# Kernel tuning notes

Measured on AMD Instinct MI355X. Metric: run time of the kernel, lower is better.

## Reference

```python
import jax, jax.numpy as jnp
import numpy as np

H, L, N = 128, 8192, 64


def setup_inputs() -> dict:
    key = jax.random.key(0)
    ks = jax.random.split(key, 8)
    u = jax.random.normal(ks[0], (H, L), jnp.float32)
    # lecun_normal-scaled params, per channel
    Ct_ri = jax.random.normal(ks[1], (H, N, 2), jnp.float32) / np.sqrt(N)
    B_raw = jax.random.normal(ks[2], (H, N, 1), jnp.float32) / np.sqrt(N)
    D = jax.random.uniform(ks[3], (H,), jnp.float32)
    lo, hi = np.log(0.001), np.log(0.1)
    log_step = jax.random.uniform(ks[4], (H,), jnp.float32) * (hi - lo) + lo
    n = np.arange(N, dtype=np.float32)
    Lambda_re = jnp.full((N,), -0.5, jnp.float32)
    Lambda_im = jnp.asarray(np.pi * n, jnp.float32)
    p_re = jnp.asarray(np.sqrt(n + 0.5), jnp.float32)
    p_im = jnp.zeros((N,), jnp.float32)
    q_re = jnp.asarray(np.sqrt(n + 0.5), jnp.float32)
    q_im = jnp.zeros((N,), jnp.float32)
    Vc_re = jax.random.normal(ks[5], (N, N), jnp.float32) / np.sqrt(N)
    Vc_im = jax.random.normal(ks[6], (N, N), jnp.float32) / np.sqrt(N)
    return dict(u=u, Ct_ri=Ct_ri, B_raw=B_raw, D=D, log_step=log_step,
                Lambda_re=Lambda_re, Lambda_im=Lambda_im,
                p_re=p_re, p_im=p_im, q_re=q_re, q_im=q_im,
                Vc_re=Vc_re, Vc_im=Vc_im)


def _s4_forward(u, Ct_ri, B_raw, D, log_step,
                Lambda_re, Lambda_im, p_re, p_im, q_re, q_im, Vc_re, Vc_im):
    h, l = u.shape
    Lambda = (Lambda_re + 1j * Lambda_im).astype(jnp.complex64)   # (N,)
    p = (p_re + 1j * p_im).astype(jnp.complex64)                  # (N,)
    q = (q_re + 1j * q_im).astype(jnp.complex64)                  # (N,)
    Vc = (Vc_re + 1j * Vc_im).astype(jnp.complex64)               # (N,N)
    Ct = (Ct_ri[..., 0] + 1j * Ct_ri[..., 1]).astype(jnp.complex64)  # (H,N)
    # B = Vc @ B_raw  per channel -> (H,N)
    B = jnp.einsum('nm,hm->hn', Vc, B_raw[..., 0].astype(jnp.complex64))
    step = jnp.exp(log_step)                                      # (H,)

    # K_gen_DPLR evaluated at the L roots of unity (conv_from_gen)
    omega = jnp.exp(-2j * jnp.pi * (jnp.arange(l) / l)).astype(jnp.complex64)  # (L,)
    g = (2.0 / step)[:, None] * ((1.0 - omega) / (1.0 + omega))[None, :]       # (H,L)
    c = 2.0 / (1.0 + omega)                                                    # (L,)

    # cauchy_dot: sum_n a_n / (g - Lambda_n); reuse one (H,L,N) reciprocal
    recip = 1.0 / (g[:, :, None] - Lambda[None, None, :])          # (H,L,N)
    Ctc = Ct.conj()
    k00 = jnp.einsum('hn,hln->hl', Ctc * B, recip)
    k01 = jnp.einsum('hn,hln->hl', Ctc * p[None, :], recip)
    k10 = jnp.einsum('hn,hln->hl', q.conj()[None, :] * B, recip)
    k11 = jnp.einsum('n,hln->hl', q.conj() * p, recip)
    at_roots = c[None, :] * (k00 - k01 * (1.0 / (1.0 + k11)) * k10)  # (H,L)

    K = jnp.fft.ifft(at_roots, n=l, axis=-1).real                 # (H,L)

    # non_circular_convolution via zero-padded rfft
    ud = jnp.fft.rfft(jnp.pad(u, ((0, 0), (0, l))), axis=-1)
    Kd = jnp.fft.rfft(jnp.pad(K, ((0, 0), (0, l))), axis=-1)
    y = jnp.fft.irfft(ud * Kd, axis=-1)[:, :l]                    # (H,L)
    return y + D[:, None] * u


def reference(u, Ct_ri, B_raw, D, log_step,
              Lambda_re, Lambda_im, p_re, p_im, q_re, q_im, Vc_re, Vc_im):
    return _s4_forward(u, Ct_ri, B_raw, D, log_step,
                       Lambda_re, Lambda_im, p_re, p_im, q_re, q_im,
                       Vc_re, Vc_im)
```

## Files before the change

### kernel.cpp

```cpp
#include <hip/hip_runtime.h>
#include <math.h>

#define H 128
#define L 8192
#define NSTATE 64
#define NTH 1024
#define PI_D 3.14159265358979323846
#define RT2 0.70710678118654752440f

#define W16K_RE 0.99999992646571789f
#define W16K_IM (-3.8349518757139556e-4f)
#define W32K_RE 0.99999998161642898f
#define W32K_IM (-1.9174759731070332e-4f)

typedef float v2f __attribute__((ext_vector_type(2)));

__device__ __forceinline__ v2f pkfma(v2f a, v2f b, v2f c) {
    return __builtin_elementwise_fma(a, b, c);
}
__device__ __forceinline__ v2f pkfma(float a, v2f b, v2f c) {
    v2f av = a; return __builtin_elementwise_fma(av, b, c);
}

__device__ __forceinline__ int SWZ(int e) { return e ^ ((e >> 3) & 7); }
__device__ __forceinline__ int TSW(int j) { return j ^ ((j >> 4) & 15) ^ ((j >> 8) & 15); }
__device__ __forceinline__ int brev13(int x) { return (int)(__brev((unsigned)x) >> 19); }

__device__ __forceinline__ float2 cmul(float2 a, float2 b) {
    return make_float2(a.x * b.x - a.y * b.y, a.x * b.y + a.y * b.x);
}
__device__ __forceinline__ float2 cmulc(float2 w, float2 x) {
    return make_float2(w.x * x.x + w.y * x.y, w.x * x.y - w.y * x.x);
}
__device__ __forceinline__ float2 cadd(float2 a, float2 b) { return make_float2(a.x + b.x, a.y + b.y); }
__device__ __forceinline__ float2 csub(float2 a, float2 b) { return make_float2(a.x - b.x, a.y - b.y); }
__device__ __forceinline__ float2 mnegi(float2 a) { return make_float2(a.y, -a.x); }
__device__ __forceinline__ float2 mposi(float2 a) { return make_float2(-a.y, a.x); }

template<int SIGMA>
__device__ __forceinline__ void dif_r8(float2* __restrict__ A,
                                       const float2* __restrict__ tw, int tid) {
    const int M1 = 1024 / SIGMA;
    int r = tid & (SIGMA - 1);
    int b = ((tid & ~(SIGMA - 1)) << 3) | r;
    float2 w1 = tw[TSW(r * M1)];
    float2 w2 = cmul(w1, w1);
    float2 w4 = cmul(w2, w2);
    float2 wj1 = cmul(w1, make_float2(RT2, -RT2));
    float2 wj2 = mnegi(w1);
    float2 wj3 = cmul(w1, make_float2(-RT2, -RT2));
    int i0 = SWZ(b), i1 = SWZ(b + SIGMA), i2 = SWZ(b + 2 * SIGMA), i3 = SWZ(b + 3 * SIGMA);
    int i4 = SWZ(b + 4 * SIGMA), i5 = SWZ(b + 5 * SIGMA), i6 = SWZ(b + 6 * SIGMA), i7 = SWZ(b + 7 * SIGMA);
    float2 x0 = A[i0], x1 = A[i1], x2 = A[i2], x3 = A[i3];
    float2 x4 = A[i4], x5 = A[i5], x6 = A[i6], x7 = A[i7];
    float2 a0 = cadd(x0, x4), a1 = cadd(x1, x5), a2 = cadd(x2, x6), a3 = cadd(x3, x7);
    float2 s0 = cmul(csub(x0, x4), w1);
    float2 s1 = cmul(csub(x1, x5), wj1);
    float2 s2 = cmul(csub(x2, x6), wj2);
    float2 s3 = cmul(csub(x3, x7), wj3);
    float2 c0 = cadd(a0, a2), c1 = cadd(a1, a3);
    float2 c2 = cmul(csub(a0, a2), w2);
    float2 c3 = cmul(mnegi(csub(a1, a3)), w2);
    float2 d0 = cadd(s0, s2), d1 = cadd(s1, s3);
    float2 d2 = cmul(csub(s0, s2), w2);
    float2 d3 = cmul(mnegi(csub(s1, s3)), w2);
    A[i0] = cadd(c0, c1); A[i1] = cmul(csub(c0, c1), w4);
    A[i2] = cadd(c2, c3); A[i3] = cmul(csub(c2, c3), w4);
    A[i4] = cadd(d0, d1); A[i5] = cmul(csub(d0, d1), w4);
    A[i6] = cadd(d2, d3); A[i7] = cmul(csub(d2, d3), w4);
}

template<int SIGMA>
__device__ __forceinline__ void dit_r8(float2* __restrict__ A,
                                       const float2* __restrict__ tw, int tid) {
    const int M1 = 1024 / SIGMA;
    int r = tid & (SIGMA - 1);
    int b = ((tid & ~(SIGMA - 1)) << 3) | r;
    float2 w1 = tw[TSW(r * M1)];
    float2 w2 = cmul(w1, w1);
    float2 w4 = cmul(w2, w2);
    float2 wj1 = cmul(w1, make_float2(RT2, -RT2));
    float2 wj2 = mnegi(w1);
    float2 wj3 = cmul(w1, make_float2(-RT2, -RT2));
    int i0 = SWZ(b), i1 = SWZ(b + SIGMA), i2 = SWZ(b + 2 * SIGMA), i3 = SWZ(b + 3 * SIGMA);
    int i4 = SWZ(b + 4 * SIGMA), i5 = SWZ(b + 5 * SIGMA), i6 = SWZ(b + 6 * SIGMA), i7 = SWZ(b + 7 * SIGMA);
    float2 x0 = A[i0], x1 = A[i1], x2 = A[i2], x3 = A[i3];
    float2 x4 = A[i4], x5 = A[i5], x6 = A[i6], x7 = A[i7];
    float2 t;
    t = cmulc(w4, x1); float2 e0 = cadd(x0, t), e1 = csub(x0, t);
    t = cmulc(w4, x3); float2 e2 = cadd(x2, t), e3 = csub(x2, t);
    t = cmulc(w4, x5); float2 e4 = cadd(x4, t), e5 = csub(x4, t);
    t = cmulc(w4, x7); float2 e6 = cadd(x6, t), e7 = csub(x6, t);
    t = cmulc(w2, e2);        float2 f0 = cadd(e0, t), f2 = csub(e0, t);
    t = mposi(cmulc(w2, e3)); float2 f1 = cadd(e1, t), f3 = csub(e1, t);
    t = cmulc(w2, e6);        float2 f4 = cadd(e4, t), f6 = csub(e4, t);
    t = mposi(cmulc(w2, e7)); float2 f5 = cadd(e5, t), f7 = csub(e5, t);
    t = cmulc(w1, f4);  A[i0] = cadd(f0, t); A[i4] = csub(f0, t);
    t = cmulc(wj1, f5); A[i1] = cadd(f1, t); A[i5] = csub(f1, t);
    t = cmulc(wj2, f6); A[i2] = cadd(f2, t); A[i6] = csub(f2, t);
    t = cmulc(wj3, f7); A[i3] = cadd(f3, t); A[i7] = csub(f3, t);
}

__device__ __forceinline__ void dif_first_load(float2* __restrict__ A,
                                               const float2* __restrict__ tw,
                                               int tid, const float* __restrict__ ur,
                                               int type) {
    #pragma unroll
    for (int rep = 0; rep < 2; ++rep) {
        int q = tid + rep * NTH;
        float u0 = ur[q], u1 = ur[q + 2048], u2v = ur[q + 4096], u3v = ur[q + 6144];
        float2 x0, x1, x2, x3;
        if (type == 0) {
            x0 = make_float2(u0, 0.f); x1 = make_float2(u1, 0.f);
            x2 = make_float2(u2v, 0.f); x3 = make_float2(u3v, 0.f);
        } else {
            int hq = q >> 1;
            float2 wa = tw[TSW(hq)];
            float2 wb = tw[TSW(hq + 1024)];
            float2 adj = (q & 1) ? make_float2(W16K_RE, W16K_IM) : make_float2(1.f, 0.f);
            wa = cmul(wa, adj); wb = cmul(wb, adj);
            float2 wc = mnegi(wa), wd = mnegi(wb);
            x0 = make_float2(u0 * wa.x, u0 * wa.y);
            x1 = make_float2(u1 * wb.x, u1 * wb.y);
            x2 = make_float2(u2v * wc.x, u2v * wc.y);
            x3 = make_float2(u3v * wd.x, u3v * wd.y);
        }
        float2 w1 = tw[TSW(q)];
        float2 w2 = cmul(w1, w1);
        float2 w1b = mnegi(w1);
        float2 y0 = cadd(x0, x2), y2 = cmul(csub(x0, x2), w1);
        float2 y1 = cadd(x1, x3), y3 = cmul(csub(x1, x3), w1b);
        A[SWZ(q)]        = cadd(y0, y1);
        A[SWZ(q + 2048)] = cmul(csub(y0, y1), w2);
        A[SWZ(q + 4096)] = cadd(y2, y3);
        A[SWZ(q + 6144)] = cmul(csub(y2, y3), w2);
    }
}

template<bool SP>
__device__ __forceinline__ void dit_last_store(const float2* __restrict__ A,
                                               const float2* __restrict__ tw,
                                               int tid, int type,
                                               const float* __restrict__ ur, float Dh,
                                               float* __restrict__ orow,
                                               float* __restrict__ yrow) {
    const float sc = 0.5f / (float)L;
    #pragma unroll
    for (int rep = 0; rep < 2; ++rep) {
        int q = tid + rep * NTH;
        float2 v1 = tw[TSW(q)];
        float2 v2 = cmul(v1, v1);
        float2 x0 = A[SWZ(q)], x1 = A[SWZ(q + 2048)];
        float2 x2 = A[SWZ(q + 4096)], x3 = A[SWZ(q + 6144)];
        float2 t1 = cmulc(v2, x1);
        float2 y0 = cadd(x0, t1), y1 = csub(x0, t1);
        float2 t3 = cmulc(v2, x3);
        float2 y2 = cadd(x2, t3), y3 = csub(x2, t3);
        float2 u2c = cmulc(v1, y2);
        float2 z0 = cadd(y0, u2c), z2 = csub(y0, u2c);
        float2 u3c = mposi(cmulc(v1, y3));
        float2 z1 = cadd(y1, u3c), z3 = csub(y1, u3c);
        float v0, vv1, vv2, vv3;
        if (type == 0) {
            v0  = z0.x * sc + Dh * ur[q];
            vv1 = z1.x * sc + Dh * ur[q + 2048];
            vv2 = z2.x * sc + Dh * ur[q + 4096];
            vv3 = z3.x * sc + Dh * ur[q + 6144];
        } else {
            int hq = q >> 1;
            float2 wa = tw[TSW(hq)];
            float2 wb = tw[TSW(hq + 1024)];
            float2 adj = (q & 1) ? make_float2(W16K_RE, W16K_IM) : make_float2(1.f, 0.f);
            wa = cmul(wa, adj); wb = cmul(wb, adj);
            float2 wc = mnegi(wa), wd = mnegi(wb);
            v0  = (wa.x * z0.x + wa.y * z0.y) * sc;
            vv1 = (wb.x * z1.x + wb.y * z1.y) * sc;
            vv2 = (wc.x * z2.x + wc.y * z2.y) * sc;
            vv3 = (wd.x * z3.x + wd.y * z3.y) * sc;
        }
        float* dst = (type == 0) ? orow : (SP ? yrow : orow);
        if constexpr (SP) {
            dst[q] = v0; dst[q + 2048] = vv1; dst[q + 4096] = vv2; dst[q + 6144] = vv3;
        } else {
            atomicAdd(&dst[q], v0); atomicAdd(&dst[q + 2048], vv1);
            atomicAdd(&dst[q + 4096], vv2); atomicAdd(&dst[q + 6144], vv3);
        }
    }
}

template<int P>
__device__ __forceinline__ void cauchy_chunk(
    const int type, const int tid, const float two_over_step,
    const float2* __restrict__ tw,
    const float4* __restrict__ wq, const float2* __restrict__ wr,
    const float4* __restrict__ wp,
    float* __restrict__ specRe, float* __restrict__ specIm)
{
    const float2 W16K = make_float2(W16K_RE, W16K_IM);
    const float2 W32K = make_float2(W32K_RE, W32K_IM);
    float tk0, tk1;
    v2f gv;
    #pragma unroll
    for (int e = 0; e < 2; ++e) {
        int k = brev13(8 * tid + 2 * P + e);
        float2 w;
        if (e == 0) {
            w = tw[TSW(k >> 1)];
        } else {
            float2 t0 = tw[TSW((k >> 1) - 2048)];
            w = make_float2(t0.y, -t0.x);
        }
        if (k & 1) w = cmul(w, W16K);
        if (type)  w = cmul(w, W32K);
        float t = -w.y * __builtin_amdgcn_rcpf(w.x);
        t = fminf(fmaxf(t, -3.0e7f), 3.0e7f);
        if (e == 0) { tk0 = t; gv.x = two_over_step * t; }
        else        { tk1 = t; gv.y = two_over_step * t; }
    }
    v2f A00x = 0.f, A00y = 0.f, A01x = 0.f, A01y = 0.f;
    v2f A10x = 0.f, A10y = 0.f, A11x = 0.f, A11y = 0.f;
    #pragma unroll 2
    for (int n = 0; n < NSTATE; ++n) {
        float4 qv = wq[n];
        float2 rv = wr[n];
        float4 pv = wp[n];
        v2f dim = gv - pv.z;
        v2f dre2 = pv.y;
        v2f den = pkfma(dim, dim, dre2);
        float rp = __builtin_amdgcn_rcpf(den.x * den.y);
        v2f inv; inv.x = den.y * rp; inv.y = den.x * rp;
        v2f rre = pv.x * inv;
        v2f rip = dim * inv;
        A00x = pkfma(qv.x, rre, pkfma( qv.y, rip, A00x));
        A00y = pkfma(qv.y, rre, pkfma(-qv.x, rip, A00y));
        A01x = pkfma(qv.z, rre, pkfma( qv.w, rip, A01x));
        A01y = pkfma(qv.w, rre, pkfma(-qv.z, rip, A01y));
        A10x = pkfma(rv.x, rre, pkfma( rv.y, rip, A10x));
        A10y = pkfma(rv.y, rre, pkfma(-rv.x, rip, A10y));
        A11x = pkfma( pv.w, rre, A11x);
        A11y = pkfma(-pv.w, rip, A11y);
    }
    #pragma unroll
    for (int e = 0; e < 2; ++e) {
        float2 a00 = make_float2(e ? A00x.y : A00x.x, e ? A00y.y : A00y.x);
        float2 a01 = make_float2(e ? A01x.y : A01x.x, e ? A01y.y : A01y.x);
        float2 a10 = make_float2(e ? A10x.y : A10x.x, e ? A10y.y : A10y.x);
        float2 a11 = make_float2(e ? A11x.y : A11x.x, e ? A11y.y : A11y.x);
        float tt = e ? tk1 : tk0;
        float2 den1 = make_float2(1.0f + a11.x, a11.y);
        float invd = 1.0f / (den1.x * den1.x + den1.y * den1.y);
        float2 qn = cmul(a01, a10);
        float2 dv = make_float2((qn.x * den1.x + qn.y * den1.y) * invd,
                                (qn.y * den1.x - qn.x * den1.y) * invd);
        float2 tmp = make_float2(a00.x - dv.x, a00.y - dv.y);
        float2 s = cmul(make_float2(1.0f, tt), tmp);
        int j = 2 * P + e;
        specRe[j * NTH + tid] = s.x;
        specIm[j * NTH + tid] = s.y;
    }
}

__global__ __launch_bounds__(NSTATE)
void s4_prep(const float* __restrict__ Ct_ri, const float* __restrict__ B_raw,
             const float* __restrict__ Lre_g, const float* __restrict__ Lim_g,
             const float* __restrict__ p_re, const float* __restrict__ p_im,
             const float* __restrict__ q_re, const float* __restrict__ q_im,
             const float* __restrict__ Vc_re, const float* __restrict__ Vc_im,
             char* __restrict__ ws)
{
    const int h = blockIdx.x, n = threadIdx.x;
    float2 Bc = make_float2(0.f, 0.f);
    for (int m = 0; m < NSTATE; ++m) {
        float br = B_raw[h * NSTATE + m];
        Bc.x += Vc_re[n * NSTATE + m] * br;
        Bc.y += Vc_im[n * NSTATE + m] * br;
    }
    float2 Ctc = make_float2(Ct_ri[(h * NSTATE + n) * 2 + 0],
                             -Ct_ri[(h * NSTATE + n) * 2 + 1]);
    float2 pc = make_float2(p_re[n], p_im[n]);
    float2 qc = make_float2(q_re[n], -q_im[n]);
    float2 w00 = cmul(Ctc, Bc);
    float2 w01 = cmul(Ctc, pc);
    float2 w10 = cmul(qc, Bc);
    float2 w11 = cmul(qc, pc);
    float dre = -Lre_g[n];
    float4* wq = (float4*)ws;
    float2* wr = (float2*)(ws + (size_t)H * NSTATE * 16);
    float4* wp = (float4*)(ws + (size_t)H * NSTATE * 24);
    wq[h * NSTATE + n] = make_float4(w00.x, w00.y, w01.x, w01.y);
    wr[h * NSTATE + n] = make_float2(w10.x, w10.y);
    wp[h * NSTATE + n] = make_float4(dre, dre * dre, Lim_g[n], w11.x);
}

__global__ __launch_bounds__(256)
void s4_combine(float4* __restrict__ out, const float4* __restrict__ yneg) {
    int i = blockIdx.x * 256 + threadIdx.x;
    float4 a = out[i], b = yneg[i];
    out[i] = make_float4(a.x + b.x, a.y + b.y, a.z + b.z, a.w + b.w);
}

extern __shared__ char smem_raw[];

template<bool WG, bool SP>
__global__ __launch_bounds__(NTH)
void s4_split_kernel(const float* __restrict__ u,
                     const float* __restrict__ Ct_ri,
                     const float* __restrict__ B_raw,
                     const float* __restrict__ Dp,
                     const float* __restrict__ log_step,
                     const float* __restrict__ Lre_g,
                     const float* __restrict__ Lim_g,
                     const float* __restrict__ p_re,
                     const float* __restrict__ p_im,
                     const float* __restrict__ q_re,
                     const float* __restrict__ q_im,
                     const float* __restrict__ Vc_re,
                     const float* __restrict__ Vc_im,
                     const char* __restrict__ wsw,
                     float* __restrict__ yneg,
                     float* __restrict__ out)
{
    float2* bufA   = (float2*)smem_raw;
    float2* tw     = bufA + L;
    float*  specRe = (float*)(tw + 2048);
    float*  specIm = specRe + L;
    float4* wq4    = (float4*)(specIm + L);
    float2* wr2    = (float2*)(wq4 + NSTATE);
    float4* wp4    = (float4*)(wr2 + NSTATE);

    const int bid  = blockIdx.x;
    const int type = bid >> 7;
    const int h    = bid & (H - 1);
    const int tid  = threadIdx.x;

    for (int j = tid; j < 2048; j += NTH) {
        double a = -2.0 * PI_D * (double)j / (double)L;
        tw[TSW(j)] = make_float2((float)cos(a), (float)sin(a));
    }
    const float4* wqp; const float2* wrp; const float4* wpp;
    if constexpr (WG) {
        wqp = (const float4*)wsw + (size_t)h * NSTATE;
        wrp = (const float2*)(wsw + (size_t)H * NSTATE * 16) + (size_t)h * NSTATE;
        wpp = (const float4*)(wsw + (size_t)H * NSTATE * 24) + (size_t)h * NSTATE;
    } else {
        if (tid < NSTATE) {
            int n = tid;
            float2 Bc = make_float2(0.f, 0.f);
            for (int m = 0; m < NSTATE; ++m) {
                float br = B_raw[h * NSTATE + m];
                Bc.x += Vc_re[n * NSTATE + m] * br;
                Bc.y += Vc_im[n * NSTATE + m] * br;
            }
            float2 Ctc = make_float2(Ct_ri[(h * NSTATE + n) * 2 + 0],
                                     -Ct_ri[(h * NSTATE + n) * 2 + 1]);
            float2 pc = make_float2(p_re[n], p_im[n]);
            float2 qc = make_float2(q_re[n], -q_im[n]);
            float2 w00 = cmul(Ctc, Bc);
            float2 w01 = cmul(Ctc, pc);
            float2 w10 = cmul(qc, Bc);
            float2 w11 = cmul(qc, pc);
            float dre = -Lre_g[n];
            wq4[n] = make_float4(w00.x, w00.y, w01.x, w01.y);
            wr2[n] = make_float2(w10.x, w10.y);
            wp4[n] = make_float4(dre, dre * dre, Lim_g[n], w11.x);
        }
        wqp = wq4; wrp = wr2; wpp = wp4;
    }
    __syncthreads();

    const float step = expf(log_step[h]);
    const float two_over_step = 2.0f / step;
    const float Dh = Dp[h];
    const float* ur = u + (size_t)h * L;

    dif_first_load(bufA, tw, tid, ur, type);
    cauchy_chunk<0>(type, tid, two_over_step, tw, wqp, wrp, wpp, specRe, specIm);
    __syncthreads();
    dif_r8<256>(bufA, tw, tid);
    cauchy_chunk<1>(type, tid, two_over_step, tw, wqp, wrp, wpp, specRe, specIm);
    __syncthreads();
    dif_r8<32>(bufA, tw, tid);
    cauchy_chunk<2>(type, tid, two_over_step, tw, wqp, wrp, wpp, specRe, specIm);
    __syncthreads();
    dif_r8<4>(bufA, tw, tid);
    cauchy_chunk<3>(type, tid, two_over_step, tw, wqp, wrp, wpp, specRe, specIm);
    __syncthreads();

    {
        const int base = tid * 8;
        #pragma unroll
        for (int un = 0; un < 2; ++un) {
            int p0 = base + un * 4;
            int j0 = SWZ(p0), j1 = SWZ(p0 + 1), j2 = SWZ(p0 + 2), j3 = SWZ(p0 + 3);
            float2 x0 = bufA[j0], x1 = bufA[j1], x2 = bufA[j2], x3 = bufA[j3];
            float2 a0 = cadd(x0, x2), a1 = cadd(x1, x3);
            float2 s0 = csub(x0, x2), s1 = mnegi(csub(x1, x3));
            float2 y0 = cadd(a0, a1), y1 = csub(a0, a1);
            float2 y2 = cadd(s0, s1), y3 = csub(s0, s1);
            int sj = un * 4;
            y0 = cmul(y0, make_float2(specRe[(sj + 0) * NTH + tid], specIm[(sj + 0) * NTH + tid]));
            y1 = cmul(y1, make_float2(specRe[(sj + 1) * NTH + tid], specIm[(sj + 1) * NTH + tid]));
            y2 = cmul(y2, make_float2(specRe[(sj + 2) * NTH + tid], specIm[(sj + 2) * NTH + tid]));
            y3 = cmul(y3, make_float2(specRe[(sj + 3) * NTH + tid], specIm[(sj + 3) * NTH + tid]));
            float2 e0 = cadd(y0, y1), e1 = csub(y0, y1);
            float2 e2 = cadd(y2, y3), e3 = csub(y2, y3);
            float2 ti = mposi(e3);
            bufA[j0] = cadd(e0, e2); bufA[j2] = csub(e0, e2);
            bufA[j1] = cadd(e1, ti); bufA[j3] = csub(e1, ti);
        }
    }
    __syncthreads();

    dit_r8<4>(bufA, tw, tid);   __syncthreads();
    dit_r8<32>(bufA, tw, tid);  __syncthreads();
    dit_r8<256>(bufA, tw, tid); __syncthreads();
    dit_last_store<SP>(bufA, tw, tid, type, ur, Dh,
                       out + (size_t)h * L,
                       SP ? (yneg + (size_t)h * L) : nullptr);
}

extern "C" void kernel_launch(void* const* d_in, const int* in_sizes, int n_in,
                              void* d_out, int out_size, void* d_ws, size_t ws_size,
                              hipStream_t stream) {
    (void)in_sizes; (void)n_in; (void)out_size;
    const float* u        = (const float*)d_in[0];
    const float* Ct_ri    = (const float*)d_in[1];
    const float* B_raw    = (const float*)d_in[2];
    const float* Dp       = (const float*)d_in[3];
    const float* log_step = (const float*)d_in[4];
    const float* Lre      = (const float*)d_in[5];
    const float* Lim      = (const float*)d_in[6];
    const float* p_re     = (const float*)d_in[7];
    const float* p_im     = (const float*)d_in[8];
    const float* q_re     = (const float*)d_in[9];
    const float* q_im     = (const float*)d_in[10];
    const float* Vc_re    = (const float*)d_in[11];
    const float* Vc_im    = (const float*)d_in[12];
    float* out = (float*)d_out;

    const size_t needW = (size_t)H * NSTATE * (16 + 8 + 16);
    const size_t needY = needW + (size_t)H * L * sizeof(float);
    const bool wg = ws_size >= needW;
    const bool sp = ws_size >= needY;

    char*  wsw  = (char*)d_ws;
    float* yneg = (float*)((char*)d_ws + needW);

    const size_t smemW = (size_t)(L + 2048) * sizeof(float2)
                       + (size_t)2 * L * sizeof(float);
    const size_t smemL = smemW + NSTATE * (16 + 8 + 16);

    if (wg) {
        s4_prep<<<dim3(H), dim3(NSTATE), 0, stream>>>(
            Ct_ri, B_raw, Lre, Lim, p_re, p_im, q_re, q_im, Vc_re, Vc_im, wsw);
        if (sp) {
            hipFuncSetAttribute((const void*)s4_split_kernel<true, true>,
                                hipFuncAttributeMaxDynamicSharedMemorySize, (int)smemW);
            s4_split_kernel<true, true><<<dim3(2 * H), dim3(NTH), smemW, stream>>>(
                u, Ct_ri, B_raw, Dp, log_step, Lre, Lim,
                p_re, p_im, q_re, q_im, Vc_re, Vc_im, wsw, yneg, out);
            s4_combine<<<dim3((H * L) / (256 * 4)), dim3(256), 0, stream>>>(
                (float4*)out, (const float4*)yneg);
        } else {
            hipMemsetAsync(out, 0, (size_t)H * L * sizeof(float), stream);
            hipFuncSetAttribute((const void*)s4_split_kernel<true, false>,
                                hipFuncAttributeMaxDynamicSharedMemorySize, (int)smemW);
            s4_split_kernel<true, false><<<dim3(2 * H), dim3(NTH), smemW, stream>>>(
                u, Ct_ri, B_raw, Dp, log_step, Lre, Lim,
                p_re, p_im, q_re, q_im, Vc_re, Vc_im, wsw, nullptr, out);
        }
    } else {
        hipMemsetAsync(out, 0, (size_t)H * L * sizeof(float), stream);
        hipFuncSetAttribute((const void*)s4_split_kernel<false, false>,
                            hipFuncAttributeMaxDynamicSharedMemorySize, (int)smemL);
        s4_split_kernel<false, false><<<dim3(2 * H), dim3(NTH), smemL, stream>>>(
            u, Ct_ri, B_raw, Dp, log_step, Lre, Lim,
            p_re, p_im, q_re, q_im, Vc_re, Vc_im, nullptr, nullptr, out);
    }
}
```

Baseline: 77.86 us.

## Restructure 8192-point FFT into radix-16/8/8/8 passes to cut LDS stages

Replaces the radix-4 first/last FFT passes plus four radix-8 passes with a radix-16 first/last pass (run by 512 threads) and radix-8 middle stages, moving the pointwise spectrum multiply into a full radix-8 butterfly. This removes one LDS round trip and one block barrier on each of the forward and inverse sides. In exchange, half the threads idle during the radix-16 passes, those threads carry 16 complex values in registers, and constant-memory twiddle tables are added.

```diff
diff --git a/kernel.cpp b/kernel.cpp
--- a/kernel.cpp
+++ b/kernel.cpp
@@ -36,6 +36,35 @@
 __device__ __forceinline__ float2 csub(float2 a, float2 b) { return make_float2(a.x - b.x, a.y - b.y); }
 __device__ __forceinline__ float2 mnegi(float2 a) { return make_float2(a.y, -a.x); }
 __device__ __forceinline__ float2 mposi(float2 a) { return make_float2(-a.y, a.x); }
+
+__device__ __constant__ float2 C16[8] = {
+    { 1.f, 0.f },
+    { 0.9238795325112867f, -0.3826834323650898f },
+    { 0.7071067811865476f, -0.7071067811865476f },
+    { 0.3826834323650898f, -0.9238795325112867f },
+    { 0.f, -1.f },
+    { -0.3826834323650898f, -0.9238795325112867f },
+    { -0.7071067811865476f, -0.7071067811865476f },
+    { -0.9238795325112867f, -0.3826834323650898f },
+};
+__device__ __constant__ float2 C32[16] = {
+    { 1.f, 0.f },
+    { 0.9807852804032304f, -0.1950903220161283f },
+    { 0.9238795325112867f, -0.3826834323650898f },
+    { 0.8314696123025452f, -0.5555702330196022f },
+    { 0.7071067811865476f, -0.7071067811865476f },
+    { 0.5555702330196022f, -0.8314696123025452f },
+    { 0.3826834323650898f, -0.9238795325112867f },
+    { 0.1950903220161283f, -0.9807852804032304f },
+    { 0.f, -1.f },
+    { -0.1950903220161283f, -0.9807852804032304f },
+    { -0.3826834323650898f, -0.9238795325112867f },
+    { -0.5555702330196022f, -0.8314696123025452f },
+    { -0.7071067811865476f, -0.7071067811865476f },
+    { -0.8314696123025452f, -0.5555702330196022f },
+    { -0.9238795325112867f, -0.3826834323650898f },
+    { -0.9807852804032304f, -0.1950903220161283f },
+};
 
 template<int SIGMA>
 __device__ __forceinline__ void dif_r8(float2* __restrict__ A,
@@ -101,89 +130,126 @@
     t = cmulc(wj3, f7); A[i3] = cadd(f3, t); A[i7] = csub(f3, t);
 }
 
-__device__ __forceinline__ void dif_first_load(float2* __restrict__ A,
-                                               const float2* __restrict__ tw,
-                                               int tid, const float* __restrict__ ur,
-                                               int type) {
-    #pragma unroll
-    for (int rep = 0; rep < 2; ++rep) {
-        int q = tid + rep * NTH;
-        float u0 = ur[q], u1 = ur[q + 2048], u2v = ur[q + 4096], u3v = ur[q + 6144];
-        float2 x0, x1, x2, x3;
-        if (type == 0) {
-            x0 = make_float2(u0, 0.f); x1 = make_float2(u1, 0.f);
-            x2 = make_float2(u2v, 0.f); x3 = make_float2(u3v, 0.f);
-        } else {
-            int hq = q >> 1;
-            float2 wa = tw[TSW(hq)];
-            float2 wb = tw[TSW(hq + 1024)];
-            float2 adj = (q & 1) ? make_float2(W16K_RE, W16K_IM) : make_float2(1.f, 0.f);
-            wa = cmul(wa, adj); wb = cmul(wb, adj);
-            float2 wc = mnegi(wa), wd = mnegi(wb);
-            x0 = make_float2(u0 * wa.x, u0 * wa.y);
-            x1 = make_float2(u1 * wb.x, u1 * wb.y);
-            x2 = make_float2(u2v * wc.x, u2v * wc.y);
-            x3 = make_float2(u3v * wd.x, u3v * wd.y);
-        }
-        float2 w1 = tw[TSW(q)];
-        float2 w2 = cmul(w1, w1);
-        float2 w1b = mnegi(w1);
-        float2 y0 = cadd(x0, x2), y2 = cmul(csub(x0, x2), w1);
-        float2 y1 = cadd(x1, x3), y3 = cmul(csub(x1, x3), w1b);
-        A[SWZ(q)]        = cadd(y0, y1);
-        A[SWZ(q + 2048)] = cmul(csub(y0, y1), w2);
-        A[SWZ(q + 4096)] = cadd(y2, y3);
-        A[SWZ(q + 6144)] = cmul(csub(y2, y3), w2);
-    }
+__device__ __forceinline__ void dif_first16(float2* __restrict__ A,
+                                            const float2* __restrict__ tw,
+                                            int t, const float* __restrict__ ur,
+                                            int type) {
+    float2 x[16];
+    if (type == 0) {
+        #pragma unroll
+        for (int j = 0; j < 16; ++j) x[j] = make_float2(ur[t + 512 * j], 0.f);
+    } else {
+        float2 wt = tw[TSW(t >> 1)];
+        if (t & 1) wt = cmul(wt, make_float2(W16K_RE, W16K_IM));
+        #pragma unroll
+        for (int j = 0; j < 16; ++j) {
+            float2 wj = cmul(wt, C32[j]);
+            float uv = ur[t + 512 * j];
+            x[j] = make_float2(uv * wj.x, uv * wj.y);
+        }
+    }
+    float2 w1 = tw[TSW(t)];
+    float2 w2 = cmul(w1, w1);
+    float2 w4 = cmul(w2, w2);
+    float2 w8 = cmul(w4, w4);
+    #pragma unroll
+    for (int j = 0; j < 8; ++j) {
+        float2 wj = cmul(w1, C16[j]);
+        float2 a = cadd(x[j], x[j + 8]);
+        float2 b = cmul(csub(x[j], x[j + 8]), wj);
+        x[j] = a; x[j + 8] = b;
+    }
+    #pragma unroll
+    for (int g = 0; g < 16; g += 8)
+        #pragma unroll
+        for (int j = 0; j < 4; ++j) {
+            float2 wj = cmul(w2, C16[2 * j]);
+            float2 a = cadd(x[g + j], x[g + j + 4]);
+            float2 b = cmul(csub(x[g + j], x[g + j + 4]), wj);
+            x[g + j] = a; x[g + j + 4] = b;
+        }
+    #pragma unroll
+    for (int g = 0; g < 16; g += 4) {
+        { float2 a = cadd(x[g], x[g + 2]);
+          float2 b = cmul(csub(x[g], x[g + 2]), w4);
+          x[g] = a; x[g + 2] = b; }
+        { float2 a = cadd(x[g + 1], x[g + 3]);
+          float2 b = cmul(csub(x[g + 1], x[g + 3]), mnegi(w4));
+          x[g + 1] = a; x[g + 3] = b; }
+    }
+    #pragma unroll
+    for (int g = 0; g < 16; g += 2) {
+        float2 a = cadd(x[g], x[g + 1]);
+        float2 b = cmul(csub(x[g], x[g + 1]), w8);
+        x[g] = a; x[g + 1] = b;
+    }
+    #pragma unroll
+    for (int j = 0; j < 16; ++j) A[SWZ(t + 512 * j)] = x[j];
 }
 
 template<bool SP>
-__device__ __forceinline__ void dit_last_store(const float2* __restrict__ A,
-                                               const float2* __restrict__ tw,
-                                               int tid, int type,
-                                               const float* __restrict__ ur, float Dh,
-                                               float* __restrict__ orow,
-                                               float* __restrict__ yrow) {
+__device__ __forceinline__ void dit_last16(const float2* __restrict__ A,
+                                           const float2* __restrict__ tw,
+                                           int t, int type,
+                                           const float* __restrict__ ur, float Dh,
+                                           float* __restrict__ orow,
+                                           float* __restrict__ yrow) {
+    float2 x[16];
+    #pragma unroll
+    for (int j = 0; j < 16; ++j) x[j] = A[SWZ(t + 512 * j)];
+    float2 w1 = tw[TSW(t)];
+    float2 w2 = cmul(w1, w1);
+    float2 w4 = cmul(w2, w2);
+    float2 w8 = cmul(w4, w4);
+    #pragma unroll
+    for (int g = 0; g < 16; g += 2) {
+        float2 tt = cmulc(w8, x[g + 1]);
+        float2 a = cadd(x[g], tt), b = csub(x[g], tt);
+        x[g] = a; x[g + 1] = b;
+    }
+    #pragma unroll
+    for (int g = 0; g < 16; g += 4) {
+        { float2 tt = cmulc(w4, x[g + 2]);
+          float2 a = cadd(x[g], tt), b = csub(x[g], tt);
+          x[g] = a; x[g + 2] = b; }
+        { float2 tt = mposi(cmulc(w4, x[g + 3]));
+          float2 a = cadd(x[g + 1], tt), b = csub(x[g + 1], tt);
+          x[g + 1] = a; x[g + 3] = b; }
+    }
+    #pragma unroll
+    for (int g = 0; g < 16; g += 8)
+        #pragma unroll
+        for (int j = 0; j < 4; ++j) {
+            float2 wj = cmul(w2, C16[2 * j]);
+            float2 tt = cmulc(wj, x[g + j + 4]);
+            float2 a = cadd(x[g + j], tt), b = csub(x[g + j], tt);
+            x[g + j] = a; x[g + j + 4] = b;
+        }
+    #pragma unroll
+    for (int j = 0; j < 8; ++j) {
+        float2 wj = cmul(w1, C16[j]);
+        float2 tt = cmulc(wj, x[j + 8]);
+        float2 a = cadd(x[j], tt), b = csub(x[j], tt);
+        x[j] = a; x[j + 8] = b;
+    }
     const float sc = 0.5f / (float)L;
-    #pragma unroll
-    for (int rep = 0; rep < 2; ++rep) {
-        int q = tid + rep * NTH;
-        float2 v1 = tw[TSW(q)];
-        float2 v2 = cmul(v1, v1);
-        float2 x0 = A[SWZ(q)], x1 = A[SWZ(q + 2048)];
-        float2 x2 = A[SWZ(q + 4096)], x3 = A[SWZ(q + 6144)];
-        float2 t1 = cmulc(v2, x1);
-        float2 y0 = cadd(x0, t1), y1 = csub(x0, t1);
-        float2 t3 = cmulc(v2, x3);
-        float2 y2 = cadd(x2, t3), y3 = csub(x2, t3);
-        float2 u2c = cmulc(v1, y2);
-        float2 z0 = cadd(y0, u2c), z2 = csub(y0, u2c);
-        float2 u3c = mposi(cmulc(v1, y3));
-        float2 z1 = cadd(y1, u3c), z3 = csub(y1, u3c);
-        float v0, vv1, vv2, vv3;
-        if (type == 0) {
-            v0  = z0.x * sc + Dh * ur[q];
-            vv1 = z1.x * sc + Dh * ur[q + 2048];
-            vv2 = z2.x * sc + Dh * ur[q + 4096];
-            vv3 = z3.x * sc + Dh * ur[q + 6144];
-        } else {
-            int hq = q >> 1;
-            float2 wa = tw[TSW(hq)];
-            float2 wb = tw[TSW(hq + 1024)];
-            float2 adj = (q & 1) ? make_float2(W16K_RE, W16K_IM) : make_float2(1.f, 0.f);
-            wa = cmul(wa, adj); wb = cmul(wb, adj);
-            float2 wc = mnegi(wa), wd = mnegi(wb);
-            v0  = (wa.x * z0.x + wa.y * z0.y) * sc;
-            vv1 = (wb.x * z1.x + wb.y * z1.y) * sc;
-            vv2 = (wc.x * z2.x + wc.y * z2.y) * sc;
-            vv3 = (wd.x * z3.x + wd.y * z3.y) * sc;
-        }
-        float* dst = (type == 0) ? orow : (SP ? yrow : orow);
-        if constexpr (SP) {
-            dst[q] = v0; dst[q + 2048] = vv1; dst[q + 4096] = vv2; dst[q + 6144] = vv3;
-        } else {
-            atomicAdd(&dst[q], v0); atomicAdd(&dst[q + 2048], vv1);
-            atomicAdd(&dst[q + 4096], vv2); atomicAdd(&dst[q + 6144], vv3);
+    if (type == 0) {
+        #pragma unroll
+        for (int j = 0; j < 16; ++j) {
+            int p = t + 512 * j;
+            float val = x[j].x * sc + Dh * ur[p];
+            if constexpr (SP) orow[p] = val; else atomicAdd(&orow[p], val);
+        }
+    } else {
+        float2 wt = tw[TSW(t >> 1)];
+        if (t & 1) wt = cmul(wt, make_float2(W16K_RE, W16K_IM));
+        float* dst = SP ? yrow : orow;
+        #pragma unroll
+        for (int j = 0; j < 16; ++j) {
+            int p = t + 512 * j;
+            float2 wj = cmul(wt, C32[j]);
+            float val = (wj.x * x[j].x + wj.y * x[j].y) * sc;
+            if constexpr (SP) dst[p] = val; else atomicAdd(&dst[p], val);
         }
     }
 }
@@ -373,48 +439,66 @@
     const float Dh = Dp[h];
     const float* ur = u + (size_t)h * L;
 
-    dif_first_load(bufA, tw, tid, ur, type);
+    if (tid < 512) dif_first16(bufA, tw, tid, ur, type);
     cauchy_chunk<0>(type, tid, two_over_step, tw, wqp, wrp, wpp, specRe, specIm);
     __syncthreads();
-    dif_r8<256>(bufA, tw, tid);
+    dif_r8<64>(bufA, tw, tid);
     cauchy_chunk<1>(type, tid, two_over_step, tw, wqp, wrp, wpp, specRe, specIm);
     __syncthreads();
-    dif_r8<32>(bufA, tw, tid);
+    dif_r8<8>(bufA, tw, tid);
     cauchy_chunk<2>(type, tid, two_over_step, tw, wqp, wrp, wpp, specRe, specIm);
-    __syncthreads();
-    dif_r8<4>(bufA, tw, tid);
     cauchy_chunk<3>(type, tid, two_over_step, tw, wqp, wrp, wpp, specRe, specIm);
     __syncthreads();
 
     {
         const int base = tid * 8;
-        #pragma unroll
-        for (int un = 0; un < 2; ++un) {
-            int p0 = base + un * 4;
-            int j0 = SWZ(p0), j1 = SWZ(p0 + 1), j2 = SWZ(p0 + 2), j3 = SWZ(p0 + 3);
-            float2 x0 = bufA[j0], x1 = bufA[j1], x2 = bufA[j2], x3 = bufA[j3];
-            float2 a0 = cadd(x0, x2), a1 = cadd(x1, x3);
-            float2 s0 = csub(x0, x2), s1 = mnegi(csub(x1, x3));
-            float2 y0 = cadd(a0, a1), y1 = csub(a0, a1);
-            float2 y2 = cadd(s0, s1), y3 = csub(s0, s1);
-            int sj = un * 4;
-            y0 = cmul(y0, make_float2(specRe[(sj + 0) * NTH + tid], specIm[(sj + 0) * NTH + tid]));
-            y1 = cmul(y1, make_float2(specRe[(sj + 1) * NTH + tid], specIm[(sj + 1) * NTH + tid]));
-            y2 = cmul(y2, make_float2(specRe[(sj + 2) * NTH + tid], specIm[(sj + 2) * NTH + tid]));
-            y3 = cmul(y3, make_float2(specRe[(sj + 3) * NTH + tid], specIm[(sj + 3) * NTH + tid]));
-            float2 e0 = cadd(y0, y1), e1 = csub(y0, y1);
-            float2 e2 = cadd(y2, y3), e3 = csub(y2, y3);
-            float2 ti = mposi(e3);
-            bufA[j0] = cadd(e0, e2); bufA[j2] = csub(e0, e2);
-            bufA[j1] = cadd(e1, ti); bufA[j3] = csub(e1, ti);
-        }
+        float2 x0 = bufA[SWZ(base + 0)], x1 = bufA[SWZ(base + 1)];
+        float2 x2 = bufA[SWZ(base + 2)], x3 = bufA[SWZ(base + 3)];
+        float2 x4 = bufA[SWZ(base + 4)], x5 = bufA[SWZ(base + 5)];
+        float2 x6 = bufA[SWZ(base + 6)], x7 = bufA[SWZ(base + 7)];
+        float2 a0 = cadd(x0, x4), a1 = cadd(x1, x5), a2 = cadd(x2, x6), a3 = cadd(x3, x7);
+        float2 s0 = csub(x0, x4), s1 = csub(x1, x5), s2 = csub(x2, x6), s3 = csub(x3, x7);
+        float2 b0 = s0;
+        float2 b1 = cmul(s1, make_float2(RT2, -RT2));
+        float2 b2 = mnegi(s2);
+        float2 b3 = cmul(s3, make_float2(-RT2, -RT2));
+        float2 c0 = cadd(a0, a2), c2 = csub(a0, a2);
+        float2 c1 = cadd(a1, a3), c3 = mnegi(csub(a1, a3));
+        float2 d0 = cadd(b0, b2), d2 = csub(b0, b2);
+        float2 d1 = cadd(b1, b3), d3 = mnegi(csub(b1, b3));
+        float2 y0 = cadd(c0, c1), y1 = csub(c0, c1);
+        float2 y2 = cadd(c2, c3), y3 = csub(c2, c3);
+        float2 y4 = cadd(d0, d1), y5 = csub(d0, d1);
+        float2 y6 = cadd(d2, d3), y7 = csub(d2, d3);
+        y0 = cmul(y0, make_float2(specRe[0 * NTH + tid], specIm[0 * NTH + tid]));
+        y1 = cmul(y1, make_float2(specRe[1 * NTH + tid], specIm[1 * NTH + tid]));
+        y2 = cmul(y2, make_float2(specRe[2 * NTH + tid], specIm[2 * NTH + tid]));
+        y3 = cmul(y3, make_float2(specRe[3 * NTH + tid], specIm[3 * NTH + tid]));
+        y4 = cmul(y4, make_float2(specRe[4 * NTH + tid], specIm[4 * NTH + tid]));
+        y5 = cmul(y5, make_float2(specRe[5 * NTH + tid], specIm[5 * NTH + tid]));
+        y6 = cmul(y6, make_float2(specRe[6 * NTH + tid], specIm[6 * NTH + tid]));
+        y7 = cmul(y7, make_float2(specRe[7 * NTH + tid], specIm[7 * NTH + tid]));
+        float2 e0 = cadd(y0, y1), e1 = csub(y0, y1), e2 = cadd(y2, y3), e3 = csub(y2, y3);
+        float2 e4 = cadd(y4, y5), e5 = csub(y4, y5), e6 = cadd(y6, y7), e7 = csub(y6, y7);
+        float2 f0 = cadd(e0, e2), f2 = csub(e0, e2);
+        float2 ti = mposi(e3); float2 f1 = cadd(e1, ti), f3 = csub(e1, ti);
+        float2 f4 = cadd(e4, e6), f6 = csub(e4, e6);
+        float2 tj = mposi(e7); float2 f5 = cadd(e5, tj), f7 = csub(e5, tj);
+        float2 g4 = f4;
+        float2 g5 = cmul(make_float2(RT2, RT2), f5);
+        float2 g6 = mposi(f6);
+        float2 g7 = cmul(make_float2(-RT2, RT2), f7);
+        bufA[SWZ(base + 0)] = cadd(f0, g4); bufA[SWZ(base + 4)] = csub(f0, g4);
+        bufA[SWZ(base + 1)] = cadd(f1, g5); bufA[SWZ(base + 5)] = csub(f1, g5);
+        bufA[SWZ(base + 2)] = cadd(f2, g6); bufA[SWZ(base + 6)] = csub(f2, g6);
+        bufA[SWZ(base + 3)] = cadd(f3, g7); bufA[SWZ(base + 7)] = csub(f3, g7);
     }
     __syncthreads();
 
-    dit_r8<4>(bufA, tw, tid);   __syncthreads();
-    dit_r8<32>(bufA, tw, tid);  __syncthreads();
-    dit_r8<256>(bufA, tw, tid); __syncthreads();
-    dit_last_store<SP>(bufA, tw, tid, type, ur, Dh,
+    dit_r8<8>(bufA, tw, tid);   __syncthreads();
+    dit_r8<64>(bufA, tw, tid);  __syncthreads();
+    if (tid < 512)
+        dit_last16<SP>(bufA, tw, tid, type, ur, Dh,
                        out + (size_t)h * L,
                        SP ? (yneg + (size_t)h * L) : nullptr);
 }
```

Measured after the change: 76.22 us. 2.1% less time.
